# Performance work log

Measured on AMD Instinct MI355X. Metric: run time of the kernel, lower is better.

## Reference

```python
import jax, jax.numpy as jnp
import numpy as np
from jax.scipy.special import logsumexp

B, D, H, L, R, K = 4096, 784, 16, 4, 4, 8
D1 = D // 2
NBIS, NNEWT = 50, 3
LOG2PI = float(np.log(2.0 * np.pi))


def square_swish(h):
    # util.square_swish nonlinearity (swish-family; see notes)
    return h * jax.nn.sigmoid(h)


def mixture_terms(xv, logits, mu, log_s):
    # xv: [B, D1]; logits/mu/log_s: [B, D1, K]
    logw = jax.nn.log_softmax(logits, axis=-1)
    t = (xv[..., None] - mu) * jnp.exp(-log_s)
    log_cdf = logsumexp(logw + jax.nn.log_sigmoid(t), axis=-1)          # log F(x)
    log_sf = logsumexp(logw + jax.nn.log_sigmoid(-t), axis=-1)          # log (1-F(x))
    log_pdf = logsumexp(logw + jax.nn.log_sigmoid(t) + jax.nn.log_sigmoid(-t) - log_s, axis=-1)  # log F'(x)
    return log_cdf, log_sf, log_pdf


def invert_mixture_logit(y, logits, mu, log_s):
    # Solve logit(F(x)) = y for x: bisection (stop-grad) + Newton polish (differentiable).
    sl, sm, ss, sy = map(jax.lax.stop_gradient, (logits, mu, log_s, y))

    def body(_, lo_hi):
        lo, hi = lo_hi
        mid = 0.5 * (lo + hi)
        lc, lsf, _ = mixture_terms(mid, sl, sm, ss)
        f = lc - lsf - sy
        return jnp.where(f < 0, mid, lo), jnp.where(f < 0, hi, mid)

    lo = jnp.full_like(y, -100.0)
    hi = jnp.full_like(y, 100.0)
    lo, hi = jax.lax.fori_loop(0, NBIS, body, (lo, hi))
    xv = jax.lax.stop_gradient(0.5 * (lo + hi))
    for _ in range(NNEWT):
        lc, lsf, lp = mixture_terms(xv, logits, mu, log_s)
        logdet = lp - lc - lsf  # d/dx logit(F(x))
        xv = xv - (lc - lsf - y) * jnp.exp(-logdet)
    lc, lsf, lp = mixture_terms(xv, logits, mu, log_s)
    return xv, lp - lc - lsf


def conditioner(h_in, Wi, bi, W1l, b1l, W2l, b2l, Wo, bo):
    h = square_swish(h_in @ Wi + bi)
    for r in range(R):  # 4 resnet blocks, hidden_dim=16
        h = h + square_swish(h @ W1l[r] + b1l[r]) @ W2l[r] + b2l[r]
    return (h @ Wo + bo).reshape(-1, D1, 3 * K)


def flow_inverse(x, eps, W_in, b_in, W1, b1, W2, b2, W_out, b_out):
    # UnitGaussianPrior sample eps -> inverse coupling stack; log q via change of variables
    log_q = -0.5 * jnp.sum(eps * eps + LOG2PI, axis=-1)
    z = eps
    for l in reversed(range(L)):
        za, zb = z[:, :D1], z[:, D1:]
        if l % 2 == 1:
            za, zb = zb, za
        p = conditioner(jnp.concatenate([zb, x], axis=-1),
                        W_in[l], b_in[l], W1[l], b1[l], W2[l], b2[l], W_out[l], b_out[l])
        logits, mu, log_s = p[..., :K], p[..., K:2 * K], p[..., 2 * K:]
        xa, ld = invert_mixture_logit(za, logits, mu, log_s)
        log_q = log_q + jnp.sum(ld, axis=-1)
        if l % 2 == 0:
            z = jnp.concatenate([xa, zb], axis=-1)
        else:
            z = jnp.concatenate([zb, xa], axis=-1)
    return z, log_q


def setup_inputs():
    key = jax.random.key(0)
    ks = jax.random.split(key, 6)
    s_in = 1.0 / np.sqrt(D1 + D)
    s_h = 1.0 / np.sqrt(H)
    return {
        "x": jax.random.normal(ks[0], (B, D), jnp.float32),
        "eps": jax.random.normal(ks[1], (B, D), jnp.float32),
        "W_in": jax.random.normal(ks[2], (L, D1 + D, H), jnp.float32) * s_in,
        "b_in": jnp.zeros((L, H), jnp.float32),
        "W1": jax.random.normal(ks[3], (L, R, H, H), jnp.float32) * s_h,
        "b1": jnp.zeros((L, R, H), jnp.float32),
        "W2": jax.random.normal(ks[4], (L, R, H, H), jnp.float32) * s_h,
        "b2": jnp.zeros((L, R, H), jnp.float32),
        "W_out": jax.random.normal(ks[5], (L, H, D1 * 3 * K), jnp.float32) * 0.05,
        "b_out": jnp.zeros((L, D1 * 3 * K), jnp.float32),
    }


def reference(x, eps, W_in, b_in, W1, b1, W2, b2, W_out, b_out):
    return flow_inverse(x, eps, W_in, b_in, W1, b1, W2, b2, W_out, b_out)
```

## Files before the change

### kernel.cpp

```cpp
#include <hip/hip_runtime.h>
#include <math.h>

constexpr int cB   = 4096;
constexpr int cD   = 784;
constexpr int cD1  = 392;
constexpr int cH   = 16;
constexpr int cL   = 4;
constexpr int cR   = 4;
constexpr int cDIN = 1176;
constexpr int cPDIM = cD1 * 3 * 8;
#define LOG2PI_F 1.8378770664093453f
#define L2E_F    1.4426950408889634f
#define LN2_F    0.6931471805599453f
#define LN_LN2_F (-0.36651292058166432701f)

__device__ __forceinline__ float rcpf(float x)  { return __builtin_amdgcn_rcpf(x); }
__device__ __forceinline__ float exp2f_(float x){ return __builtin_amdgcn_exp2f(x); }
__device__ __forceinline__ float log2f_(float x){ return __builtin_amdgcn_logf(x); }
__device__ __forceinline__ float expn(float x)  { return exp2f_(x * L2E_F); }
__device__ __forceinline__ float logn(float x)  { return log2f_(x) * LN2_F; }

typedef __attribute__((ext_vector_type(2))) float f32x2;

__global__ void __launch_bounds__(256, 4) mlp_kernel(
    const float* __restrict__ zbsrc, const float* __restrict__ x,
    const float* __restrict__ Win, const float* __restrict__ bin,
    const float* __restrict__ W1, const float* __restrict__ b1,
    const float* __restrict__ W2, const float* __restrict__ b2,
    float* __restrict__ hbuf,
    const float* __restrict__ eps, float* __restrict__ logq, int do_init)
{
    __shared__ float part[4][4][16];
    const int wid  = threadIdx.x >> 6;
    const int lane = threadIdx.x & 63;
    const int j = lane & 15;
    const int G = lane >> 4;
    const int bs = blockIdx.x * 4;
    const int r0 = wid * 294;

    if (do_init) {
        const int b = bs + wid;
        const float4* e = (const float4*)(eps + (size_t)b * cD);
        float sum = 0.f;
        for (int i = lane; i < cD / 4; i += 64) {
            float4 v = e[i];
            sum = fmaf(v.x, v.x, sum); sum = fmaf(v.y, v.y, sum);
            sum = fmaf(v.z, v.z, sum); sum = fmaf(v.w, v.w, sum);
        }
        #pragma unroll
        for (int off = 32; off; off >>= 1) sum += __shfl_xor(sum, off, 64);
        if (lane == 0) logq[b] = -0.5f * sum - 0.5f * (float)cD * LOG2PI_F;
    }

    float acc[4][16];
    #pragma unroll
    for (int s = 0; s < 4; ++s)
        #pragma unroll
        for (int c = 0; c < 16; ++c) acc[s][c] = 0.f;

    const float* pz[4]; const float* px[4];
    #pragma unroll
    for (int s = 0; s < 4; ++s) {
        pz[s] = zbsrc + (size_t)(bs + s) * cD;
        px[s] = x + (size_t)(bs + s) * cD - cD1;
    }

    for (int i = r0 + lane; i < r0 + 294; i += 64) {
        const float4* wr = (const float4*)(Win + (size_t)i * cH);
        float4 w0 = wr[0], w1 = wr[1], w2 = wr[2], w3 = wr[3];
        float wv[16] = {w0.x,w0.y,w0.z,w0.w, w1.x,w1.y,w1.z,w1.w,
                        w2.x,w2.y,w2.z,w2.w, w3.x,w3.y,w3.z,w3.w};
        #pragma unroll
        for (int s = 0; s < 4; ++s) {
            const float* src = (i < cD1) ? pz[s] : px[s];
            float v = src[i];
            #pragma unroll
            for (int c = 0; c < 16; ++c) acc[s][c] = fmaf(v, wv[c], acc[s][c]);
        }
    }

    #pragma unroll
    for (int s = 0; s < 4; ++s) {
        #pragma unroll
        for (int c = 0; c < 8; ++c) {
            float sent = (lane & 8) ? acc[s][c] : acc[s][c + 8];
            float mine = (lane & 8) ? acc[s][c + 8] : acc[s][c];
            acc[s][c] = mine + __shfl_xor(sent, 8, 64);
        }
        #pragma unroll
        for (int c = 0; c < 4; ++c) {
            float sent = (lane & 4) ? acc[s][c] : acc[s][c + 4];
            float mine = (lane & 4) ? acc[s][c + 4] : acc[s][c];
            acc[s][c] = mine + __shfl_xor(sent, 4, 64);
        }
        #pragma unroll
        for (int c = 0; c < 2; ++c) {
            float sent = (lane & 2) ? acc[s][c] : acc[s][c + 2];
            float mine = (lane & 2) ? acc[s][c + 2] : acc[s][c];
            acc[s][c] = mine + __shfl_xor(sent, 2, 64);
        }
        {
            float sent = (lane & 1) ? acc[s][0] : acc[s][1];
            float mine = (lane & 1) ? acc[s][1] : acc[s][0];
            acc[s][0] = mine + __shfl_xor(sent, 1, 64);
        }
    }
    const int g4 = (lane >> 4) & 1, g5 = (lane >> 5) & 1;
    float a01, a23, colsum;
    {
        float sent = g4 ? acc[0][0] : acc[1][0];
        float keep = g4 ? acc[1][0] : acc[0][0];
        a01 = keep + __shfl_xor(sent, 16, 64);
    }
    {
        float sent = g4 ? acc[2][0] : acc[3][0];
        float keep = g4 ? acc[3][0] : acc[2][0];
        a23 = keep + __shfl_xor(sent, 16, 64);
    }
    {
        float sent = g5 ? a01 : a23;
        float keep = g5 ? a23 : a01;
        colsum = keep + __shfl_xor(sent, 32, 64);
    }

    part[wid][G][j] = colsum;
    __syncthreads();
    if (wid != 0) return;

    colsum = part[0][G][j] + part[1][G][j] + part[2][G][j] + part[3][G][j];

    float t0 = colsum + bin[j];
    float hj = t0 * rcpf(1.0f + expn(-t0));

    #pragma unroll
    for (int r = 0; r < cR; ++r) {
        const float* w1r = W1 + r * 256;
        const float* w2r = W2 + r * 256;
        float u = b1[r * 16 + j];
        #pragma unroll
        for (int i = 0; i < 16; ++i)
            u = fmaf(__shfl(hj, i, 16), w1r[i * 16 + j], u);
        u = u * rcpf(1.0f + expn(-u));
        float v = b2[r * 16 + j];
        #pragma unroll
        for (int i = 0; i < 16; ++i)
            v = fmaf(__shfl(u, i, 16), w2r[i * 16 + j], v);
        hj += v;
    }
    hbuf[(size_t)j * cB + (bs + G)] = hj;
}

__global__ void __launch_bounds__(256) invert_kernel(
    float* __restrict__ z, const float* __restrict__ ysrc,
    const float* __restrict__ hbuf,
    const float* __restrict__ Wo, const float* __restrict__ bo,
    float* __restrict__ logq, int za_off)
{
    __shared__ __align__(16) float WoS[16][96];
    __shared__ float hhS[16][64];
    __shared__ float red[256];

    const int tid  = threadIdx.x;
    const int wid  = tid >> 6;
    const int lane = tid & 63;
    const int colbase = blockIdx.x * 96;
    const int b0 = blockIdx.y * 64;

    #pragma unroll
    for (int t = 0; t < 6; ++t) {
        int idx = tid + t * 256;
        int r = idx / 96, c = idx - r * 96;
        WoS[r][c] = Wo[(size_t)r * cPDIM + colbase + c];
    }
    #pragma unroll
    for (int t = 0; t < 4; ++t) {
        int idx = tid + t * 256;
        int i = idx >> 6, bb = idx & 63;
        hhS[i][bb] = hbuf[(size_t)i * cB + b0 + bb];
    }

    const int d = __builtin_amdgcn_readfirstlane(blockIdx.x * 4 + wid);
    const int b = b0 + lane;

    const float y0  = ysrc[(size_t)b * cD + za_off + d];

    __syncthreads();

    f32x2 P[12];
    {
        const f32x2* bp = (const f32x2*)(bo + (size_t)d * 24);
        #pragma unroll
        for (int j2 = 0; j2 < 12; ++j2) P[j2] = bp[j2];
        #pragma unroll
        for (int i = 0; i < 16; ++i) {
            const float hv = hhS[i][lane];
            const f32x2 hv2 = {hv, hv};
            const float4* wr = (const float4*)&WoS[i][wid * 24];
            #pragma unroll
            for (int q = 0; q < 6; ++q) {
                float4 wv = wr[q];
                f32x2 wa = {wv.x, wv.y};
                f32x2 wb = {wv.z, wv.w};
                P[2*q]   = __builtin_elementwise_fma(hv2, wa, P[2*q]);
                P[2*q+1] = __builtin_elementwise_fma(hv2, wb, P[2*q+1]);
            }
        }
    }

    const float sgn = (y0 < 0.f) ? -1.f : 1.f;
    const float yb  = fabsf(y0);

    f32x2 pm2[4], q22[4], wt2[4], is22[4], nm22[4];
    float S, lgSn, SLN2, lo, hi, x0;
    {
        float m = P[0][0];
        #pragma unroll
        for (int k = 1; k < 8; ++k) m = fmaxf(m, P[k >> 1][k & 1]);
        S = 0.f;
        #pragma unroll
        for (int k = 0; k < 8; ++k) {
            float pmv = P[k >> 1][k & 1] - m;
            float wtv = exp2f_(pmv * L2E_F);
            pm2[k >> 1][k & 1] = pmv;
            wt2[k >> 1][k & 1] = wtv;
            S += wtv;
        }
        lgSn = log2f_(S) * LN2_F;
        SLN2 = S * LN2_F;
        float lo0 = 1e30f, hi0 = -1e30f, xa = 0.f;
        #pragma unroll
        for (int k = 0; k < 8; ++k) {
            float q2v = P[8 + (k >> 1)][k & 1] * L2E_F;
            float sk  = exp2f_(q2v);
            float ik  = exp2f_(-q2v);
            float is2v = ik * L2E_F;
            float mub = sgn * P[4 + (k >> 1)][k & 1];
            q22[k >> 1][k & 1]  = q2v;
            is22[k >> 1][k & 1] = is2v;
            nm22[k >> 1][k & 1] = -mub * is2v;
            float wtv = wt2[k >> 1][k & 1];
            float inv = fmaf(yb, sk, mub);
            lo0 = fminf(lo0, inv); hi0 = fmaxf(hi0, inv);
            xa = fmaf(wtv, inv, xa);
        }
        float pad = 1e-3f + 1e-5f * (fabsf(lo0) + fabsf(hi0));
        lo = lo0 - pad; hi = hi0 + pad;
        x0 = xa * rcpf(S);
    }

    float xv, ld;
    if (yb <= 30.0f) {
        xv = x0;
        #pragma unroll 1
        for (int it = 0; it < 3; ++it) {
            f32x2 xv2 = {xv, xv};
            f32x2 sfv2 = {0.f, 0.f}, pdfa2 = {0.f, 0.f};
            #pragma unroll
            for (int kk = 0; kk < 4; ++kk) {
                f32x2 t2 = __builtin_elementwise_fma(xv2, is22[kk], nm22[kk]);
                f32x2 e1;
                e1.x = 1.0f + exp2f_(t2.x);
                e1.y = 1.0f + exp2f_(t2.y);
                f32x2 r = { rcpf(e1.x), rcpf(e1.y) };
                sfv2  = __builtin_elementwise_fma(wt2[kk], r, sfv2);
                f32x2 rr = __builtin_elementwise_fma(-r, r, r);
                f32x2 wis2v = wt2[kk] * is22[kk];
                pdfa2 = __builtin_elementwise_fma(wis2v, rr, pdfa2);
            }
            float sfv = sfv2.x + sfv2.y;
            float pdfa = pdfa2.x + pdfa2.y;
            float cdf = S - sfv;
            float f = (log2f_(cdf) - log2f_(sfv)) * LN2_F;
            if (f < yb) lo = xv; else hi = xv;
            float step = (f - yb) * cdf * sfv * rcpf(pdfa * SLN2);
            float xn = xv - step;
            if (!(xn > lo && xn < hi)) xn = 0.5f * (lo + hi);
            xv = xn;
        }
        {
            f32x2 xv2 = {xv, xv};
            f32x2 sfv2 = {0.f, 0.f}, pdfa2 = {0.f, 0.f};
            #pragma unroll
            for (int kk = 0; kk < 4; ++kk) {
                f32x2 t2 = __builtin_elementwise_fma(xv2, is22[kk], nm22[kk]);
                f32x2 e1;
                e1.x = 1.0f + exp2f_(t2.x);
                e1.y = 1.0f + exp2f_(t2.y);
                f32x2 r = { rcpf(e1.x), rcpf(e1.y) };
                sfv2  = __builtin_elementwise_fma(wt2[kk], r, sfv2);
                f32x2 rr = __builtin_elementwise_fma(-r, r, r);
                f32x2 wis2v = wt2[kk] * is22[kk];
                pdfa2 = __builtin_elementwise_fma(wis2v, rr, pdfa2);
            }
            float sfv = sfv2.x + sfv2.y;
            float pdfa = pdfa2.x + pdfa2.y;
            float cdf = S - sfv;
            float l2c = log2f_(cdf), l2s = log2f_(sfv), l2p = log2f_(pdfa);
            ld = (l2p - l2c - l2s) * LN2_F + LN_LN2_F + lgSn;
            float f = (l2c - l2s) * LN2_F;
            if (f < yb) lo = xv; else hi = xv;
            float step = (f - yb) * cdf * sfv * rcpf(pdfa * SLN2);
            float xn = xv - step;
            if (!(xn > lo && xn < hi)) xn = 0.5f * (lo + hi);
            xv = xn;
        }
    } else {
        xv = x0;
        #pragma unroll 1
        for (int it = 0; it < 4; ++it) {
            float u[8];
            float mu_ = -1e30f;
            #pragma unroll
            for (int k = 0; k < 8; ++k) {
                float is2v = is22[k >> 1][k & 1];
                float nm2v = nm22[k >> 1][k & 1];
                float lwv  = pm2[k >> 1][k & 1] - lgSn;
                float t  = fmaf(xv, is2v, nm2v) * LN2_F;
                float ec = fminf(expn(-t), 1.0f);
                u[k] = lwv - t - ec * fmaf(-0.5f, ec, 1.0f);
                mu_ = fmaxf(mu_, u[k]);
            }
            float Su = 0.f;
            #pragma unroll
            for (int k = 0; k < 8; ++k) Su += expn(u[k] - mu_);
            float lsf = mu_ + logn(Su);
            float m2 = -1e30f;
            #pragma unroll
            for (int k = 0; k < 8; ++k) m2 = fmaxf(m2, u[k] - q22[k >> 1][k & 1] * LN2_F);
            float S2 = 0.f;
            #pragma unroll
            for (int k = 0; k < 8; ++k) S2 += expn(u[k] - q22[k >> 1][k & 1] * LN2_F - m2);
            float lp = m2 + logn(S2);
            if (it == 3) { ld = lp - lsf; break; }
            float f = -lsf;
            if (f < yb) lo = xv; else hi = xv;
            float step = (f - yb) * expn(lsf - lp);
            float xn = xv - step;
            if (!(xn > lo && xn < hi)) xn = 0.5f * (lo + hi);
            xv = xn;
        }
    }

    z[(size_t)b * cD + za_off + d] = sgn * xv;

    red[tid] = ld;
    __syncthreads();
    if (wid == 0) {
        float ssum = red[lane] + red[lane + 64] + red[lane + 128] + red[lane + 192];
        atomicAdd(&logq[b], ssum);
    }
}

extern "C" void kernel_launch(void* const* d_in, const int* in_sizes, int n_in,
                              void* d_out, int out_size, void* d_ws, size_t ws_size,
                              hipStream_t stream) {
    const float* x     = (const float*)d_in[0];
    const float* eps   = (const float*)d_in[1];
    const float* W_in  = (const float*)d_in[2];
    const float* b_in  = (const float*)d_in[3];
    const float* W1    = (const float*)d_in[4];
    const float* b1    = (const float*)d_in[5];
    const float* W2    = (const float*)d_in[6];
    const float* b2    = (const float*)d_in[7];
    const float* W_out = (const float*)d_in[8];
    const float* b_out = (const float*)d_in[9];

    float* z    = (float*)d_out;
    float* logq = z + (size_t)cB * cD;
    float* hbuf = (float*)d_ws;

    for (int l = cL - 1; l >= 0; --l) {
        const int zb_off = (l & 1) ? 0 : cD1;
        const int za_off = (l & 1) ? cD1 : 0;
        const float* zbsrc = (l == 3) ? (eps + zb_off) : (z + zb_off);
        const float* ysrc  = (l >= 2) ? eps : z;
        mlp_kernel<<<cB / 4, 256, 0, stream>>>(
            zbsrc, x,
            W_in + (size_t)l * cDIN * cH, b_in + (size_t)l * cH,
            W1 + (size_t)l * cR * cH * cH, b1 + (size_t)l * cR * cH,
            W2 + (size_t)l * cR * cH * cH, b2 + (size_t)l * cR * cH,
            hbuf,
            eps, logq, (l == 3) ? 1 : 0);
        invert_kernel<<<dim3(cD1 / 4, cB / 64), 256, 0, stream>>>(
            z, ysrc, hbuf,
            W_out + (size_t)l * cH * cPDIM, b_out + (size_t)l * cPDIM,
            logq, za_off);
    }
}
```

Measured before the change: 297.6 us.

## Process two batch rows per thread with a fast Newton path for moderate targets

```diff
diff --git a/kernel.cpp b/kernel.cpp
--- a/kernel.cpp
+++ b/kernel.cpp
@@ -150,41 +150,15 @@
     hbuf[(size_t)j * cB + (bs + G)] = hj;
 }
 
-__global__ void __launch_bounds__(256) invert_kernel(
-    float* __restrict__ z, const float* __restrict__ ysrc,
-    const float* __restrict__ hbuf,
-    const float* __restrict__ Wo, const float* __restrict__ bo,
-    float* __restrict__ logq, int za_off)
+__device__ void solve_full(int b, int d, float y0,
+                           const float* __restrict__ hbuf,
+                           const float* __restrict__ Wo,
+                           const float* __restrict__ bo,
+                           float& xv_out, float& ld_out, float& sgn_out)
 {
-    __shared__ __align__(16) float WoS[16][96];
-    __shared__ float hhS[16][64];
-    __shared__ float red[256];
-
-    const int tid  = threadIdx.x;
-    const int wid  = tid >> 6;
-    const int lane = tid & 63;
-    const int colbase = blockIdx.x * 96;
-    const int b0 = blockIdx.y * 64;
-
-    #pragma unroll
-    for (int t = 0; t < 6; ++t) {
-        int idx = tid + t * 256;
-        int r = idx / 96, c = idx - r * 96;
-        WoS[r][c] = Wo[(size_t)r * cPDIM + colbase + c];
-    }
-    #pragma unroll
-    for (int t = 0; t < 4; ++t) {
-        int idx = tid + t * 256;
-        int i = idx >> 6, bb = idx & 63;
-        hhS[i][bb] = hbuf[(size_t)i * cB + b0 + bb];
-    }
-
-    const int d = __builtin_amdgcn_readfirstlane(blockIdx.x * 4 + wid);
-    const int b = b0 + lane;
-
-    const float y0  = ysrc[(size_t)b * cD + za_off + d];
-
-    __syncthreads();
+    float hh[16];
+    #pragma unroll
+    for (int i = 0; i < 16; ++i) hh[i] = hbuf[(size_t)i * cB + b];
 
     f32x2 P[12];
     {
@@ -193,9 +167,8 @@
         for (int j2 = 0; j2 < 12; ++j2) P[j2] = bp[j2];
         #pragma unroll
         for (int i = 0; i < 16; ++i) {
-            const float hv = hhS[i][lane];
-            const f32x2 hv2 = {hv, hv};
-            const float4* wr = (const float4*)&WoS[i][wid * 24];
+            const f32x2 hv2 = {hh[i], hh[i]};
+            const float4* wr = (const float4*)(Wo + (size_t)i * cPDIM + (size_t)d * 24);
             #pragma unroll
             for (int q = 0; q < 6; ++q) {
                 float4 wv = wr[q];
@@ -209,6 +182,7 @@
 
     const float sgn = (y0 < 0.f) ? -1.f : 1.f;
     const float yb  = fabsf(y0);
+    sgn_out = sgn;
 
     f32x2 pm2[4], q22[4], wt2[4], is22[4], nm22[4];
     float S, lgSn, SLN2, lo, hi, x0;
@@ -340,14 +314,190 @@
             xv = xn;
         }
     }
-
-    z[(size_t)b * cD + za_off + d] = sgn * xv;
-
-    red[tid] = ld;
+    xv_out = xv;
+    ld_out = ld;
+}
+
+__global__ void __launch_bounds__(256) invert_kernel(
+    float* __restrict__ z, const float* __restrict__ ysrc,
+    const float* __restrict__ hbuf,
+    const float* __restrict__ Wo, const float* __restrict__ bo,
+    float* __restrict__ logq, int za_off)
+{
+    __shared__ float red[2][256];
+    const int wid  = threadIdx.x >> 6;
+    const int lane = threadIdx.x & 63;
+    const int d = __builtin_amdgcn_readfirstlane(blockIdx.x * 4 + wid);
+    const int b0 = blockIdx.y * 128;
+    const int b[2] = { b0 + lane, b0 + 64 + lane };
+
+    float hh[2][16];
+    #pragma unroll
+    for (int i = 0; i < 16; ++i) {
+        hh[0][i] = hbuf[(size_t)i * cB + b[0]];
+        hh[1][i] = hbuf[(size_t)i * cB + b[1]];
+    }
+    float y0[2];
+    y0[0] = ysrc[(size_t)b[0] * cD + za_off + d];
+    y0[1] = ysrc[(size_t)b[1] * cD + za_off + d];
+
+    f32x2 P[2][12];
+    {
+        const f32x2* bp = (const f32x2*)(bo + (size_t)d * 24);
+        #pragma unroll
+        for (int j2 = 0; j2 < 12; ++j2) { P[0][j2] = bp[j2]; P[1][j2] = P[0][j2]; }
+        #pragma unroll
+        for (int i = 0; i < 16; ++i) {
+            const float4* wr = (const float4*)(Wo + (size_t)i * cPDIM + (size_t)d * 24);
+            float4 w[6];
+            #pragma unroll
+            for (int q = 0; q < 6; ++q) w[q] = wr[q];
+            #pragma unroll
+            for (int m = 0; m < 2; ++m) {
+                const f32x2 hv2 = {hh[m][i], hh[m][i]};
+                #pragma unroll
+                for (int q = 0; q < 6; ++q) {
+                    f32x2 wa = {w[q].x, w[q].y};
+                    f32x2 wb = {w[q].z, w[q].w};
+                    P[m][2*q]   = __builtin_elementwise_fma(hv2, wa, P[m][2*q]);
+                    P[m][2*q+1] = __builtin_elementwise_fma(hv2, wb, P[m][2*q+1]);
+                }
+            }
+        }
+    }
+
+    float sgn[2], yb[2];
+    #pragma unroll
+    for (int m = 0; m < 2; ++m) {
+        sgn[m] = (y0[m] < 0.f) ? -1.f : 1.f;
+        yb[m]  = fabsf(y0[m]);
+    }
+
+    float xv[2], ld[2];
+    const bool fast = (yb[0] <= 30.0f) && (yb[1] <= 30.0f);
+    if (fast) {
+        f32x2 wt2[2][4], is22[2][4], nm22[2][4];
+        float S[2], lgSn[2], SLN2[2], lo[2], hi[2];
+        #pragma unroll
+        for (int m = 0; m < 2; ++m) {
+            float mx = P[m][0][0];
+            #pragma unroll
+            for (int k = 1; k < 8; ++k) mx = fmaxf(mx, P[m][k >> 1][k & 1]);
+            float Sv = 0.f;
+            #pragma unroll
+            for (int k = 0; k < 8; ++k) {
+                float pmv = P[m][k >> 1][k & 1] - mx;
+                float wtv = exp2f_(pmv * L2E_F);
+                wt2[m][k >> 1][k & 1] = wtv;
+                Sv += wtv;
+            }
+            S[m] = Sv;
+            lgSn[m] = log2f_(Sv) * LN2_F;
+            SLN2[m] = Sv * LN2_F;
+            float lo0 = 1e30f, hi0 = -1e30f, xa = 0.f;
+            #pragma unroll
+            for (int k = 0; k < 8; ++k) {
+                float q2v = P[m][8 + (k >> 1)][k & 1] * L2E_F;
+                float sk  = exp2f_(q2v);
+                float ik  = exp2f_(-q2v);
+                float is2v = ik * L2E_F;
+                float mub = sgn[m] * P[m][4 + (k >> 1)][k & 1];
+                is22[m][k >> 1][k & 1] = is2v;
+                nm22[m][k >> 1][k & 1] = -mub * is2v;
+                float wtv = wt2[m][k >> 1][k & 1];
+                float inv = fmaf(yb[m], sk, mub);
+                lo0 = fminf(lo0, inv); hi0 = fmaxf(hi0, inv);
+                xa = fmaf(wtv, inv, xa);
+            }
+            float pad = 1e-3f + 1e-5f * (fabsf(lo0) + fabsf(hi0));
+            lo[m] = lo0 - pad; hi[m] = hi0 + pad;
+            xv[m] = xa * rcpf(S[m]);
+        }
+
+        #pragma unroll 1
+        for (int it = 0; it < 3; ++it) {
+            float sfv[2], pdfa[2];
+            #pragma unroll
+            for (int m = 0; m < 2; ++m) {
+                f32x2 xv2 = {xv[m], xv[m]};
+                f32x2 sfv2 = {0.f, 0.f}, pdfa2 = {0.f, 0.f};
+                #pragma unroll
+                for (int kk = 0; kk < 4; ++kk) {
+                    f32x2 t2 = __builtin_elementwise_fma(xv2, is22[m][kk], nm22[m][kk]);
+                    f32x2 e1;
+                    e1.x = 1.0f + exp2f_(t2.x);
+                    e1.y = 1.0f + exp2f_(t2.y);
+                    f32x2 r = { rcpf(e1.x), rcpf(e1.y) };
+                    sfv2  = __builtin_elementwise_fma(wt2[m][kk], r, sfv2);
+                    f32x2 rr = __builtin_elementwise_fma(-r, r, r);
+                    f32x2 wis2v = wt2[m][kk] * is22[m][kk];
+                    pdfa2 = __builtin_elementwise_fma(wis2v, rr, pdfa2);
+                }
+                sfv[m]  = sfv2.x + sfv2.y;
+                pdfa[m] = pdfa2.x + pdfa2.y;
+            }
+            #pragma unroll
+            for (int m = 0; m < 2; ++m) {
+                float cdf = S[m] - sfv[m];
+                float f = (log2f_(cdf) - log2f_(sfv[m])) * LN2_F;
+                if (f < yb[m]) lo[m] = xv[m]; else hi[m] = xv[m];
+                float step = (f - yb[m]) * cdf * sfv[m] * rcpf(pdfa[m] * SLN2[m]);
+                float xn = xv[m] - step;
+                if (!(xn > lo[m] && xn < hi[m])) xn = 0.5f * (lo[m] + hi[m]);
+                xv[m] = xn;
+            }
+        }
+        {
+            float sfv[2], pdfa[2];
+            #pragma unroll
+            for (int m = 0; m < 2; ++m) {
+                f32x2 xv2 = {xv[m], xv[m]};
+                f32x2 sfv2 = {0.f, 0.f}, pdfa2 = {0.f, 0.f};
+                #pragma unroll
+                for (int kk = 0; kk < 4; ++kk) {
+                    f32x2 t2 = __builtin_elementwise_fma(xv2, is22[m][kk], nm22[m][kk]);
+                    f32x2 e1;
+                    e1.x = 1.0f + exp2f_(t2.x);
+                    e1.y = 1.0f + exp2f_(t2.y);
+                    f32x2 r = { rcpf(e1.x), rcpf(e1.y) };
+                    sfv2  = __builtin_elementwise_fma(wt2[m][kk], r, sfv2);
+                    f32x2 rr = __builtin_elementwise_fma(-r, r, r);
+                    f32x2 wis2v = wt2[m][kk] * is22[m][kk];
+                    pdfa2 = __builtin_elementwise_fma(wis2v, rr, pdfa2);
+                }
+                sfv[m]  = sfv2.x + sfv2.y;
+                pdfa[m] = pdfa2.x + pdfa2.y;
+            }
+            #pragma unroll
+            for (int m = 0; m < 2; ++m) {
+                float cdf = S[m] - sfv[m];
+                float l2c = log2f_(cdf), l2s = log2f_(sfv[m]), l2p = log2f_(pdfa[m]);
+                ld[m] = (l2p - l2c - l2s) * LN2_F + LN_LN2_F + lgSn[m];
+                float f = (l2c - l2s) * LN2_F;
+                if (f < yb[m]) lo[m] = xv[m]; else hi[m] = xv[m];
+                float step = (f - yb[m]) * cdf * sfv[m] * rcpf(pdfa[m] * SLN2[m]);
+                float xn = xv[m] - step;
+                if (!(xn > lo[m] && xn < hi[m])) xn = 0.5f * (lo[m] + hi[m]);
+                xv[m] = xn;
+            }
+        }
+    } else {
+        #pragma unroll 1
+        for (int m = 0; m < 2; ++m)
+            solve_full(b[m], d, y0[m], hbuf, Wo, bo, xv[m], ld[m], sgn[m]);
+    }
+
+    z[(size_t)b[0] * cD + za_off + d] = sgn[0] * xv[0];
+    z[(size_t)b[1] * cD + za_off + d] = sgn[1] * xv[1];
+
+    red[0][threadIdx.x] = ld[0];
+    red[1][threadIdx.x] = ld[1];
     __syncthreads();
     if (wid == 0) {
-        float ssum = red[lane] + red[lane + 64] + red[lane + 128] + red[lane + 192];
-        atomicAdd(&logq[b], ssum);
+        float s0 = red[0][lane] + red[0][lane + 64] + red[0][lane + 128] + red[0][lane + 192];
+        atomicAdd(&logq[b0 + lane], s0);
+        float s1 = red[1][lane] + red[1][lane + 64] + red[1][lane + 128] + red[1][lane + 192];
+        atomicAdd(&logq[b0 + 64 + lane], s1);
     }
 }
 
@@ -381,7 +531,7 @@
             W2 + (size_t)l * cR * cH * cH, b2 + (size_t)l * cR * cH,
             hbuf,
             eps, logq, (l == 3) ? 1 : 0);
-        invert_kernel<<<dim3(cD1 / 4, cB / 64), 256, 0, stream>>>(
+        invert_kernel<<<dim3(cD1 / 4, cB / 128), 256, 0, stream>>>(
             z, ysrc, hbuf,
             W_out + (size_t)l * cH * cPDIM, b_out + (size_t)l * cPDIM,
             logq, za_off);
```

Result: no change. 300.7 us (+1.0%).
